# Kernel tuning notes

Measured on AMD Instinct MI355X. Metric: run time of the kernel, lower is better.

The kernel has to match this reference:

```python
import jax, jax.numpy as jnp
import numpy as np

BETA = 1.0
K = 2.5
IOU_THRESH = 0.4


def point_form(boxes):
    # center form (cx, cy, w, h) -> corner form (xmin, ymin, xmax, ymax)
    return jnp.concatenate([boxes[:, :2] - boxes[:, 2:] / 2,
                            boxes[:, :2] + boxes[:, 2:] / 2], axis=1)


def jaccard(box_a, box_b):
    # box_a: [T,4], box_b: [P,4] corner form -> IoU [T,P]
    lt = jnp.maximum(box_a[:, None, :2], box_b[None, :, :2])
    rb = jnp.minimum(box_a[:, None, 2:], box_b[None, :, 2:])
    wh = jnp.clip(rb - lt, 0.0)
    inter = wh[..., 0] * wh[..., 1]  # [T,P]
    area_a = ((box_a[:, 2] - box_a[:, 0]) * (box_a[:, 3] - box_a[:, 1]))[:, None]
    area_b = ((box_b[:, 2] - box_b[:, 0]) * (box_b[:, 3] - box_b[:, 1]))[None, :]
    return inter / (area_a + area_b - inter)


def setup_inputs() -> dict:
    key = jax.random.key(0)
    k1, k2, k3, k4 = jax.random.split(key, 4)
    P, T = 262144, 128
    locs = jax.random.uniform(k1, (P, 2), dtype=jnp.float32)  # prior centers
    # params: (w, h, alpha_logit); keep w,h positive and modest
    wh = jax.random.uniform(k2, (P, 2), dtype=jnp.float32) * 0.2 + 0.02
    alpha = jax.random.normal(k3, (P, 1), dtype=jnp.float32)
    params = jnp.concatenate([wh, alpha], axis=1)
    # truths in corner form with positive extent
    t_cxcy = jax.random.uniform(k4, (T, 2), dtype=jnp.float32)
    t_wh = jax.random.uniform(jax.random.fold_in(key, 7), (T, 2), dtype=jnp.float32) * 0.3 + 0.1
    truths = jnp.concatenate([t_cxcy - t_wh / 2, t_cxcy + t_wh / 2], axis=1)
    # ensure every prior overlaps at least one truth (avoids log(0) degeneracy)
    truths = truths.at[0].set(jnp.array([0.0, 0.0, 1.0, 1.0], dtype=jnp.float32))
    return {"locs": locs, "params": params, "truths": truths}


def reference(locs, params, truths):
    sigmoid_alphas = jax.nn.sigmoid(params[:, -1])           # [P]
    priors = jnp.concatenate([locs, params[:, :2]], axis=1)  # [P,4] center form
    overlaps = jaccard(truths, point_form(priors))           # [T,P]
    best_truth_overlap = overlaps.max(axis=0)                # [P]
    best_prior_overlap = overlaps.max(axis=1)                # [T]
    best_prior_idx = overlaps.argmax(axis=1)                 # [T]
    best_truth_overlap = best_truth_overlap.at[best_prior_idx].set(best_prior_overlap)
    x_filter = jnp.where(best_truth_overlap > IOU_THRESH, 1.0, 0.0)
    x_filter = x_filter.at[best_prior_idx].set(K)
    loss = (-(sigmoid_alphas * x_filter * jnp.log(best_truth_overlap)).sum()
            + BETA * sigmoid_alphas.sum()) / x_filter.sum()
    return loss
```

## Files before the change

### kernel.cpp

```cpp
#include <hip/hip_runtime.h>

#define T_CNT   128
#define IOU_TH  0.4f
#define K_CONST 2.5f
#define NB_A    512
#define NB_B    1024
#define PPT     2
#define CB      256

static const size_t WS_ACC_OFF    = 0;
static const size_t WS_PACKED_OFF = 64;
static const size_t WS_BTO_OFF    = 4096;

__global__ __launch_bounds__(256) void apb_work(
    const float* __restrict__ locs, const float* __restrict__ params,
    const float* __restrict__ truths, float* __restrict__ bto,
    unsigned long long* __restrict__ packed, double* __restrict__ accum)
{
    const int tid = threadIdx.x;

    if (blockIdx.x < NB_A) {
        __shared__ float4 s_tb[T_CNT];
        __shared__ float  s_red[3][4];

        if (tid < T_CNT) s_tb[tid] = ((const float4*)truths)[tid];
        __syncthreads();

        const int base = blockIdx.x * (256 * PPT);

        float px1[PPT], py1[PPT], px2[PPT], py2[PPT], parea[PPT];
#pragma unroll
        for (int k = 0; k < PPT; ++k) {
            int p = base + k * 256 + tid;
            float2 c = ((const float2*)locs)[p];
            float w = params[3 * p];
            float h = params[3 * p + 1];
            px1[k] = c.x - 0.5f * w; py1[k] = c.y - 0.5f * h;
            px2[k] = c.x + 0.5f * w; py2[k] = c.y + 0.5f * h;
            parea[k] = (px2[k] - px1[k]) * (py2[k] - py1[k]);
        }

        float btmax[PPT];
#pragma unroll
        for (int k = 0; k < PPT; ++k) btmax[k] = 0.f;

#pragma unroll 2
        for (int t = 0; t < T_CNT; ++t) {
            float4 tb = s_tb[t];
            float ta = (tb.z - tb.x) * (tb.w - tb.y);
#pragma unroll
            for (int k = 0; k < PPT; ++k) {
                float lx = fmaxf(tb.x, px1[k]);
                float ly = fmaxf(tb.y, py1[k]);
                float rx = fminf(tb.z, px2[k]);
                float ry = fminf(tb.w, py2[k]);
                float w = fmaxf(rx - lx, 0.f);
                float h = fmaxf(ry - ly, 0.f);
                float inter = w * h;
                float iou = inter * __builtin_amdgcn_rcpf((ta + parea[k]) - inter);
                btmax[k] = fmaxf(btmax[k], iou);
            }
        }

        float s1 = 0.f, s2 = 0.f, s3 = 0.f;
#pragma unroll
        for (int k = 0; k < PPT; ++k) {
            int p = base + k * 256 + tid;
            float a = params[3 * p + 2];
            float sig = 1.f / (1.f + expf(-a));
            float bt = btmax[k];
            float xf = (bt > IOU_TH) ? 1.f : 0.f;
            s1 += sig;
            s2 += xf;
            s3 += (xf > 0.f) ? sig * logf(bt) : 0.f;
            bto[p] = bt;
        }
#pragma unroll
        for (int off = 32; off; off >>= 1) {
            s1 += __shfl_xor(s1, off, 64);
            s2 += __shfl_xor(s2, off, 64);
            s3 += __shfl_xor(s3, off, 64);
        }
        const int wv = tid >> 6;
        if ((tid & 63) == 0) { s_red[0][wv] = s1; s_red[1][wv] = s2; s_red[2][wv] = s3; }
        __syncthreads();
        if (tid == 0) {
            atomicAdd(&accum[0], (double)(s_red[0][0] + s_red[0][1] + s_red[0][2] + s_red[0][3]));
            atomicAdd(&accum[1], (double)(s_red[1][0] + s_red[1][1] + s_red[1][2] + s_red[1][3]));
            atomicAdd(&accum[2], (double)(s_red[2][0] + s_red[2][1] + s_red[2][2] + s_red[2][3]));
        }
    } else {
        __shared__ float4 s_p[CB];
        __shared__ unsigned long long s_part[4][T_CNT];

        const int base = (blockIdx.x - NB_A) * CB;
        {
            int p = base + tid;
            float2 c = ((const float2*)locs)[p];
            float w = params[3 * p];
            float h = params[3 * p + 1];
            s_p[tid] = make_float4(c.x - 0.5f * w, c.y - 0.5f * h,
                                   c.x + 0.5f * w, c.y + 0.5f * h);
        }
        const int lane = tid & 63;
        float4 t0 = ((const float4*)truths)[lane];
        float4 t1 = ((const float4*)truths)[64 + lane];
        float ta0 = (t0.z - t0.x) * (t0.w - t0.y);
        float ta1 = (t1.z - t1.x) * (t1.w - t1.y);
        __syncthreads();

        const int wv = tid >> 6;
        const int wbase = wv * (CB / 4);
        float maxv0 = -1.f, maxv1 = -1.f;
        unsigned int maxi0 = 0u, maxi1 = 0u;

#pragma unroll 4
        for (int j = 0; j < CB / 4; ++j) {
            float4 pb = s_p[wbase + j];
            float parea = (pb.z - pb.x) * (pb.w - pb.y);
            unsigned int pg = (unsigned int)(base + wbase + j);
            {
                float lx = fmaxf(t0.x, pb.x);
                float ly = fmaxf(t0.y, pb.y);
                float rx = fminf(t0.z, pb.z);
                float ry = fminf(t0.w, pb.w);
                float w = fmaxf(rx - lx, 0.f);
                float h = fmaxf(ry - ly, 0.f);
                float inter = w * h;
                float iou = inter * __builtin_amdgcn_rcpf((ta0 + parea) - inter);
                if (iou > maxv0) { maxv0 = iou; maxi0 = pg; }
            }
            {
                float lx = fmaxf(t1.x, pb.x);
                float ly = fmaxf(t1.y, pb.y);
                float rx = fminf(t1.z, pb.z);
                float ry = fminf(t1.w, pb.w);
                float w = fmaxf(rx - lx, 0.f);
                float h = fmaxf(ry - ly, 0.f);
                float inter = w * h;
                float iou = inter * __builtin_amdgcn_rcpf((ta1 + parea) - inter);
                if (iou > maxv1) { maxv1 = iou; maxi1 = pg; }
            }
        }

        s_part[wv][lane] =
            ((unsigned long long)__float_as_uint(maxv0) << 32) |
            (unsigned long long)(~maxi0);
        s_part[wv][64 + lane] =
            ((unsigned long long)__float_as_uint(maxv1) << 32) |
            (unsigned long long)(~maxi1);
        __syncthreads();

        if (tid < T_CNT) {
            unsigned long long m = s_part[0][tid];
            unsigned long long a = s_part[1][tid];
            unsigned long long b = s_part[2][tid];
            unsigned long long c = s_part[3][tid];
            m = (a > m) ? a : m;
            m = (b > m) ? b : m;
            m = (c > m) ? c : m;
            atomicMax(&packed[tid], m);
        }
    }
}

__global__ __launch_bounds__(128) void apb_final(
    const float* __restrict__ params, const float* __restrict__ bto,
    const unsigned long long* __restrict__ packed,
    const double* __restrict__ accum, float* __restrict__ out)
{
    const int t = threadIdx.x;
    __shared__ unsigned int s_idx[T_CNT];

    unsigned long long v = packed[t];
    float ov = __uint_as_float((unsigned int)(v >> 32));
    unsigned int p = ~(unsigned int)(v & 0xFFFFFFFFull);
    s_idx[t] = p;
    __syncthreads();

    bool is_last = true;
    for (int u = t + 1; u < T_CNT; ++u)
        if (s_idx[u] == p) is_last = false;

    float c2 = 0.f, c3 = 0.f;
    if (is_last && v != 0ull) {
        float old = bto[p];
        float oxf = (old > IOU_TH) ? 1.f : 0.f;
        float a = params[3 * p + 2];
        float sig = 1.f / (1.f + expf(-a));
        float oldterm = (oxf > 0.f) ? sig * logf(old) : 0.f;
        float newterm = K_CONST * sig * logf(ov);
        c3 = newterm - oldterm;
        c2 = K_CONST - oxf;
    }

#pragma unroll
    for (int off = 32; off; off >>= 1) {
        c2 += __shfl_xor(c2, off, 64);
        c3 += __shfl_xor(c3, off, 64);
    }
    __shared__ float sw[4];
    if ((t & 63) == 0) { sw[(t >> 6) * 2] = c2; sw[(t >> 6) * 2 + 1] = c3; }
    __syncthreads();

    if (t == 0) {
        double S1 = accum[0];
        double S2 = accum[1] + (double)(sw[0] + sw[2]);
        double S3 = accum[2] + (double)(sw[1] + sw[3]);
        out[0] = (float)((S1 - S3) / S2);
    }
}

extern "C" void kernel_launch(void* const* d_in, const int* in_sizes, int n_in,
                              void* d_out, int out_size, void* d_ws, size_t ws_size,
                              hipStream_t stream) {
    const float* locs   = (const float*)d_in[0];
    const float* params = (const float*)d_in[1];
    const float* truths = (const float*)d_in[2];

    double* accum = (double*)((char*)d_ws + WS_ACC_OFF);
    unsigned long long* packed = (unsigned long long*)((char*)d_ws + WS_PACKED_OFF);
    float* bto = (float*)((char*)d_ws + WS_BTO_OFF);

    hipMemsetAsync(d_ws, 0, 1088, stream);

    apb_work<<<NB_A + NB_B, 256, 0, stream>>>(locs, params, truths, bto, packed, accum);
    apb_final<<<1, 128, 0, stream>>>(params, bto, packed, accum, (float*)d_out);
}
```

Before: 54.35 us.

## Fuse column-max and row-argmax passes into one IoU pass with DPP wave reductions

The two separate block types, one computing each prior's best truth overlap and one computing each truth's best prior, are merged into a single kernel. It computes each IoU once and derives both reductions from it. The per-prior max across the 128 truths held by lanes uses a DPP cross-lane max followed by a readlane, and the result is kept in the lane matching the prior index. This halves the IoU arithmetic but adds a six-step DPP reduction and a readlane per inner iteration, which may serialize the loop.

```diff
diff --git a/kernel.cpp b/kernel.cpp
--- a/kernel.cpp
+++ b/kernel.cpp
@@ -3,164 +3,136 @@
 #define T_CNT   128
 #define IOU_TH  0.4f
 #define K_CONST 2.5f
-#define NB_A    512
-#define NB_B    1024
-#define PPT     2
-#define CB      256
+#define PPB     256
 
 static const size_t WS_ACC_OFF    = 0;
 static const size_t WS_PACKED_OFF = 64;
 static const size_t WS_BTO_OFF    = 4096;
 
-__global__ __launch_bounds__(256) void apb_work(
+__device__ inline float wave_max_dpp(float m) {
+    int t;
+    t = __builtin_amdgcn_update_dpp(__float_as_int(m), __float_as_int(m), 0x111, 0xf, 0xf, false);
+    m = fmaxf(m, __int_as_float(t));
+    t = __builtin_amdgcn_update_dpp(__float_as_int(m), __float_as_int(m), 0x112, 0xf, 0xf, false);
+    m = fmaxf(m, __int_as_float(t));
+    t = __builtin_amdgcn_update_dpp(__float_as_int(m), __float_as_int(m), 0x114, 0xf, 0xf, false);
+    m = fmaxf(m, __int_as_float(t));
+    t = __builtin_amdgcn_update_dpp(__float_as_int(m), __float_as_int(m), 0x118, 0xf, 0xf, false);
+    m = fmaxf(m, __int_as_float(t));
+    t = __builtin_amdgcn_update_dpp(__float_as_int(m), __float_as_int(m), 0x142, 0xa, 0xf, false);
+    m = fmaxf(m, __int_as_float(t));
+    t = __builtin_amdgcn_update_dpp(__float_as_int(m), __float_as_int(m), 0x143, 0xc, 0xf, false);
+    m = fmaxf(m, __int_as_float(t));
+    return m;
+}
+
+__global__ __launch_bounds__(256) void apb_single(
     const float* __restrict__ locs, const float* __restrict__ params,
     const float* __restrict__ truths, float* __restrict__ bto,
     unsigned long long* __restrict__ packed, double* __restrict__ accum)
 {
-    const int tid = threadIdx.x;
-
-    if (blockIdx.x < NB_A) {
-        __shared__ float4 s_tb[T_CNT];
-        __shared__ float  s_red[3][4];
-
-        if (tid < T_CNT) s_tb[tid] = ((const float4*)truths)[tid];
-        __syncthreads();
-
-        const int base = blockIdx.x * (256 * PPT);
-
-        float px1[PPT], py1[PPT], px2[PPT], py2[PPT], parea[PPT];
+    __shared__ float4 s_p[PPB];
+    __shared__ unsigned long long s_part[4][T_CNT];
+    __shared__ float s_red[3][4];
+
+    const int tid  = threadIdx.x;
+    const int lane = tid & 63;
+    const int wv   = tid >> 6;
+    const int base = blockIdx.x * PPB;
+
+    {
+        int p = base + tid;
+        float2 c = ((const float2*)locs)[p];
+        float w = params[3 * p];
+        float h = params[3 * p + 1];
+        s_p[tid] = make_float4(c.x - 0.5f * w, c.y - 0.5f * h,
+                               c.x + 0.5f * w, c.y + 0.5f * h);
+    }
+    float4 t0 = ((const float4*)truths)[lane];
+    float4 t1 = ((const float4*)truths)[64 + lane];
+    float ta0 = (t0.z - t0.x) * (t0.w - t0.y);
+    float ta1 = (t1.z - t1.x) * (t1.w - t1.y);
+    __syncthreads();
+
+    const int wbase = wv * 64;
+    float maxv0 = -1.f, maxv1 = -1.f;
+    unsigned int maxi0 = 0u, maxi1 = 0u;
+    unsigned int b_bto = 0u;
+
+#pragma unroll 4
+    for (int j = 0; j < 64; ++j) {
+        float4 pb = s_p[wbase + j];
+        float parea = (pb.z - pb.x) * (pb.w - pb.y);
+        unsigned int pg = (unsigned int)(base + wbase + j);
+
+        float iou0, iou1;
+        {
+            float lx = fmaxf(t0.x, pb.x);
+            float ly = fmaxf(t0.y, pb.y);
+            float rx = fminf(t0.z, pb.z);
+            float ry = fminf(t0.w, pb.w);
+            float w = fmaxf(rx - lx, 0.f);
+            float h = fmaxf(ry - ly, 0.f);
+            float inter = w * h;
+            iou0 = inter * __builtin_amdgcn_rcpf((ta0 + parea) - inter);
+        }
+        {
+            float lx = fmaxf(t1.x, pb.x);
+            float ly = fmaxf(t1.y, pb.y);
+            float rx = fminf(t1.z, pb.z);
+            float ry = fminf(t1.w, pb.w);
+            float w = fmaxf(rx - lx, 0.f);
+            float h = fmaxf(ry - ly, 0.f);
+            float inter = w * h;
+            iou1 = inter * __builtin_amdgcn_rcpf((ta1 + parea) - inter);
+        }
+        if (iou0 > maxv0) { maxv0 = iou0; maxi0 = pg; }
+        if (iou1 > maxv1) { maxv1 = iou1; maxi1 = pg; }
+
+        float m = wave_max_dpp(fmaxf(iou0, iou1));
+        int r = __builtin_amdgcn_readlane(__float_as_int(m), 63);
+        if (lane == j) b_bto = (unsigned int)r;
+    }
+
+    s_part[wv][lane] =
+        ((unsigned long long)__float_as_uint(maxv0) << 32) |
+        (unsigned long long)(~maxi0);
+    s_part[wv][64 + lane] =
+        ((unsigned long long)__float_as_uint(maxv1) << 32) |
+        (unsigned long long)(~maxi1);
+
+    const int q = base + wbase + lane;
+    const float bt = __uint_as_float(b_bto);
+    bto[q] = bt;
+    float a = params[3 * q + 2];
+    float sig = 1.f / (1.f + expf(-a));
+    float xf = (bt > IOU_TH) ? 1.f : 0.f;
+    float s1 = sig;
+    float s2 = xf;
+    float s3 = (xf > 0.f) ? sig * logf(bt) : 0.f;
 #pragma unroll
-        for (int k = 0; k < PPT; ++k) {
-            int p = base + k * 256 + tid;
-            float2 c = ((const float2*)locs)[p];
-            float w = params[3 * p];
-            float h = params[3 * p + 1];
-            px1[k] = c.x - 0.5f * w; py1[k] = c.y - 0.5f * h;
-            px2[k] = c.x + 0.5f * w; py2[k] = c.y + 0.5f * h;
-            parea[k] = (px2[k] - px1[k]) * (py2[k] - py1[k]);
-        }
-
-        float btmax[PPT];
-#pragma unroll
-        for (int k = 0; k < PPT; ++k) btmax[k] = 0.f;
-
-#pragma unroll 2
-        for (int t = 0; t < T_CNT; ++t) {
-            float4 tb = s_tb[t];
-            float ta = (tb.z - tb.x) * (tb.w - tb.y);
-#pragma unroll
-            for (int k = 0; k < PPT; ++k) {
-                float lx = fmaxf(tb.x, px1[k]);
-                float ly = fmaxf(tb.y, py1[k]);
-                float rx = fminf(tb.z, px2[k]);
-                float ry = fminf(tb.w, py2[k]);
-                float w = fmaxf(rx - lx, 0.f);
-                float h = fmaxf(ry - ly, 0.f);
-                float inter = w * h;
-                float iou = inter * __builtin_amdgcn_rcpf((ta + parea[k]) - inter);
-                btmax[k] = fmaxf(btmax[k], iou);
-            }
-        }
-
-        float s1 = 0.f, s2 = 0.f, s3 = 0.f;
-#pragma unroll
-        for (int k = 0; k < PPT; ++k) {
-            int p = base + k * 256 + tid;
-            float a = params[3 * p + 2];
-            float sig = 1.f / (1.f + expf(-a));
-            float bt = btmax[k];
-            float xf = (bt > IOU_TH) ? 1.f : 0.f;
-            s1 += sig;
-            s2 += xf;
-            s3 += (xf > 0.f) ? sig * logf(bt) : 0.f;
-            bto[p] = bt;
-        }
-#pragma unroll
-        for (int off = 32; off; off >>= 1) {
-            s1 += __shfl_xor(s1, off, 64);
-            s2 += __shfl_xor(s2, off, 64);
-            s3 += __shfl_xor(s3, off, 64);
-        }
-        const int wv = tid >> 6;
-        if ((tid & 63) == 0) { s_red[0][wv] = s1; s_red[1][wv] = s2; s_red[2][wv] = s3; }
-        __syncthreads();
-        if (tid == 0) {
-            atomicAdd(&accum[0], (double)(s_red[0][0] + s_red[0][1] + s_red[0][2] + s_red[0][3]));
-            atomicAdd(&accum[1], (double)(s_red[1][0] + s_red[1][1] + s_red[1][2] + s_red[1][3]));
-            atomicAdd(&accum[2], (double)(s_red[2][0] + s_red[2][1] + s_red[2][2] + s_red[2][3]));
-        }
-    } else {
-        __shared__ float4 s_p[CB];
-        __shared__ unsigned long long s_part[4][T_CNT];
-
-        const int base = (blockIdx.x - NB_A) * CB;
-        {
-            int p = base + tid;
-            float2 c = ((const float2*)locs)[p];
-            float w = params[3 * p];
-            float h = params[3 * p + 1];
-            s_p[tid] = make_float4(c.x - 0.5f * w, c.y - 0.5f * h,
-                                   c.x + 0.5f * w, c.y + 0.5f * h);
-        }
-        const int lane = tid & 63;
-        float4 t0 = ((const float4*)truths)[lane];
-        float4 t1 = ((const float4*)truths)[64 + lane];
-        float ta0 = (t0.z - t0.x) * (t0.w - t0.y);
-        float ta1 = (t1.z - t1.x) * (t1.w - t1.y);
-        __syncthreads();
-
-        const int wv = tid >> 6;
-        const int wbase = wv * (CB / 4);
-        float maxv0 = -1.f, maxv1 = -1.f;
-        unsigned int maxi0 = 0u, maxi1 = 0u;
-
-#pragma unroll 4
-        for (int j = 0; j < CB / 4; ++j) {
-            float4 pb = s_p[wbase + j];
-            float parea = (pb.z - pb.x) * (pb.w - pb.y);
-            unsigned int pg = (unsigned int)(base + wbase + j);
-            {
-                float lx = fmaxf(t0.x, pb.x);
-                float ly = fmaxf(t0.y, pb.y);
-                float rx = fminf(t0.z, pb.z);
-                float ry = fminf(t0.w, pb.w);
-                float w = fmaxf(rx - lx, 0.f);
-                float h = fmaxf(ry - ly, 0.f);
-                float inter = w * h;
-                float iou = inter * __builtin_amdgcn_rcpf((ta0 + parea) - inter);
-                if (iou > maxv0) { maxv0 = iou; maxi0 = pg; }
-            }
-            {
-                float lx = fmaxf(t1.x, pb.x);
-                float ly = fmaxf(t1.y, pb.y);
-                float rx = fminf(t1.z, pb.z);
-                float ry = fminf(t1.w, pb.w);
-                float w = fmaxf(rx - lx, 0.f);
-                float h = fmaxf(ry - ly, 0.f);
-                float inter = w * h;
-                float iou = inter * __builtin_amdgcn_rcpf((ta1 + parea) - inter);
-                if (iou > maxv1) { maxv1 = iou; maxi1 = pg; }
-            }
-        }
-
-        s_part[wv][lane] =
-            ((unsigned long long)__float_as_uint(maxv0) << 32) |
-            (unsigned long long)(~maxi0);
-        s_part[wv][64 + lane] =
-            ((unsigned long long)__float_as_uint(maxv1) << 32) |
-            (unsigned long long)(~maxi1);
-        __syncthreads();
-
-        if (tid < T_CNT) {
-            unsigned long long m = s_part[0][tid];
-            unsigned long long a = s_part[1][tid];
-            unsigned long long b = s_part[2][tid];
-            unsigned long long c = s_part[3][tid];
-            m = (a > m) ? a : m;
-            m = (b > m) ? b : m;
-            m = (c > m) ? c : m;
-            atomicMax(&packed[tid], m);
-        }
+    for (int off = 32; off; off >>= 1) {
+        s1 += __shfl_xor(s1, off, 64);
+        s2 += __shfl_xor(s2, off, 64);
+        s3 += __shfl_xor(s3, off, 64);
+    }
+    if (lane == 0) { s_red[0][wv] = s1; s_red[1][wv] = s2; s_red[2][wv] = s3; }
+    __syncthreads();
+
+    if (tid < T_CNT) {
+        unsigned long long m = s_part[0][tid];
+        unsigned long long x1 = s_part[1][tid];
+        unsigned long long x2 = s_part[2][tid];
+        unsigned long long x3 = s_part[3][tid];
+        m = (x1 > m) ? x1 : m;
+        m = (x2 > m) ? x2 : m;
+        m = (x3 > m) ? x3 : m;
+        atomicMax(&packed[tid], m);
+    }
+    if (tid == 0) {
+        atomicAdd(&accum[0], (double)(s_red[0][0] + s_red[0][1] + s_red[0][2] + s_red[0][3]));
+        atomicAdd(&accum[1], (double)(s_red[1][0] + s_red[1][1] + s_red[1][2] + s_red[1][3]));
+        atomicAdd(&accum[2], (double)(s_red[2][0] + s_red[2][1] + s_red[2][2] + s_red[2][3]));
     }
 }
 
@@ -217,13 +189,14 @@
     const float* locs   = (const float*)d_in[0];
     const float* params = (const float*)d_in[1];
     const float* truths = (const float*)d_in[2];
+    const int P = in_sizes[0] / 2;
 
     double* accum = (double*)((char*)d_ws + WS_ACC_OFF);
     unsigned long long* packed = (unsigned long long*)((char*)d_ws + WS_PACKED_OFF);
     float* bto = (float*)((char*)d_ws + WS_BTO_OFF);
 
-    hipMemsetAsync(d_ws, 0, 1088, stream);
-
-    apb_work<<<NB_A + NB_B, 256, 0, stream>>>(locs, params, truths, bto, packed, accum);
+    (void)hipMemsetAsync(d_ws, 0, 1088, stream);
+
+    apb_single<<<P / PPB, 256, 0, stream>>>(locs, params, truths, bto, packed, accum);
     apb_final<<<1, 128, 0, stream>>>(params, bto, packed, accum, (float*)d_out);
 }
```

Measured after the change: 65.60 us. 20.7% more time.
